# Optimization experiments

Measured on AMD Instinct MI355X. Metric: run time of the kernel, lower is better.

## Reference

```python
import jax, jax.numpy as jnp
import numpy as np

N, E, B = 4096, 4096, 128  # nodes, edges, graphs


def _param(key, shape, scale):
    return jax.random.normal(key, shape, dtype=jnp.float32) * scale


def setup_inputs() -> dict:
    key = jax.random.key(0)
    ks = jax.random.split(key, 32)
    inp = {
        "x": jax.random.normal(ks[0], (N, 37), dtype=jnp.float32),
        "edge_index": jax.random.randint(ks[1], (2, E), 0, N),
        "edge_attr": jax.random.uniform(ks[2], (E, 5), dtype=jnp.float32),
        "batch": jnp.sort(jax.random.randint(ks[3], (N,), 0, B)),
        # NNConv 1: edge-MLP 5->512->37*128, root [37,128]
        "nn1_w1": _param(ks[4], (5, 512), 0.3),
        "nn1_b1": jnp.zeros((512,), jnp.float32),
        "nn1_w2": _param(ks[5], (512, 37 * 128), 0.01),
        "nn1_b2": jnp.zeros((37 * 128,), jnp.float32),
        "root1": _param(ks[6], (37, 128), 0.1),
        "bias1": jnp.zeros((128,), jnp.float32),
        # NNConv 2: edge-MLP 5->128->128*256, root [128,256]
        "nn2_w1": _param(ks[7], (5, 128), 0.3),
        "nn2_b1": jnp.zeros((128,), jnp.float32),
        "nn2_w2": _param(ks[8], (128, 128 * 256), 0.005),
        "nn2_b2": jnp.zeros((128 * 256,), jnp.float32),
        "root2": _param(ks[9], (128, 256), 0.05),
        "bias2": jnp.zeros((256,), jnp.float32),
        # NNConv 3: edge-MLP 5->128->256*256, root [256,256]
        "nn3_w1": _param(ks[10], (5, 128), 0.3),
        "nn3_b1": jnp.zeros((128,), jnp.float32),
        "nn3_w2": _param(ks[11], (128, 256 * 256), 0.005),
        "nn3_b2": jnp.zeros((256 * 256,), jnp.float32),
        "root3": _param(ks[12], (256, 256), 0.05),
        "bias3": jnp.zeros((256,), jnp.float32),
        # readout MLP
        "fc1_w": _param(ks[13], (256, 128), 0.06),
        "fc1_b": jnp.zeros((128,), jnp.float32),
        "fc2_w": _param(ks[14], (128, 64), 0.09),
        "fc2_b": jnp.zeros((64,), jnp.float32),
        "fc3_w": _param(ks[15], (64, 1), 0.12),
        "fc3_b": jnp.zeros((1,), jnp.float32),
    }
    return inp


def _nnconv(x, src, dst, edge_attr, w1, b1, w2, b2, root, bias, cin, cout):
    # edge MLP -> per-edge weight matrix [E, cin, cout]
    h = jax.nn.relu(edge_attr @ w1 + b1)
    W = (h @ w2 + b2).reshape(-1, cin, cout)
    # gather source features, per-edge matvec, scatter-add to targets
    msg = jnp.einsum('ei,eio->eo', x[src], W)          # [E, cout]
    agg = jax.ops.segment_sum(msg, dst, num_segments=x.shape[0])
    return agg + x @ root + bias


def _segment_mean(x, seg, num_segments):
    s = jax.ops.segment_sum(x, seg, num_segments=num_segments)
    cnt = jax.ops.segment_sum(jnp.ones((x.shape[0],), x.dtype), seg,
                              num_segments=num_segments)
    return s / jnp.maximum(cnt, 1.0)[:, None]


def reference(x, edge_index, edge_attr, batch,
              nn1_w1, nn1_b1, nn1_w2, nn1_b2, root1, bias1,
              nn2_w1, nn2_b1, nn2_w2, nn2_b2, root2, bias2,
              nn3_w1, nn3_b1, nn3_w2, nn3_b2, root3, bias3,
              fc1_w, fc1_b, fc2_w, fc2_b, fc3_w, fc3_b):
    src, dst = edge_index[0], edge_index[1]
    h = jax.nn.elu(_nnconv(x, src, dst, edge_attr, nn1_w1, nn1_b1, nn1_w2,
                           nn1_b2, root1, bias1, 37, 128))
    h = jax.nn.elu(_nnconv(h, src, dst, edge_attr, nn2_w1, nn2_b1, nn2_w2,
                           nn2_b2, root2, bias2, 128, 256))
    h = jax.nn.elu(_nnconv(h, src, dst, edge_attr, nn3_w1, nn3_b1, nn3_w2,
                           nn3_b2, root3, bias3, 256, 256))
    g = _segment_mean(h, batch, B)                     # [B, 256]
    g = jax.nn.elu(g @ fc1_w + fc1_b)
    g = jax.nn.elu(g @ fc2_w + fc2_b)
    g = g @ fc3_w + fc3_b
    return g.reshape(-1)
```

## Files before the change

### kernel.cpp

```cpp
#include <hip/hip_runtime.h>
#include <cstdint>
#include <cstddef>

typedef float f32x4 __attribute__((ext_vector_type(4)));
typedef _Float16 f16x8 __attribute__((ext_vector_type(8)));
typedef _Float16 f16x4 __attribute__((ext_vector_type(4)));

__device__ __forceinline__ float elu_f(float x) { return x > 0.f ? x : expm1f(x); }

__device__ __forceinline__ void gload_lds16(const void* g, void* l)
{
    __builtin_amdgcn_global_load_lds(
        (const __attribute__((address_space(1))) void*)g,
        (__attribute__((address_space(3))) void*)l,
        16, 0, 0);
}

template <int CIN, int COUT, int KFTOT>
__device__ __forceinline__
void pack_body(int bid, int tid, const float* __restrict__ w2, const float* __restrict__ b2,
               _Float16* __restrict__ w2h, int KH, float* tile )
{
    const int kh = bid / KFTOT;
    const int c  = bid - kh * KFTOT;
    const int CP = 32 * COUT;
    for (int i = tid; i < CP; i += 256) {
        int kk = i / COUT, n = i - kk * COUT;
        int kg = c * 32 + kk;
        float v = 0.f;
        if (kg < CIN) v = (kh < KH) ? w2[((size_t)kh * CIN + kg) * COUT + n]
                                    : b2[(size_t)kg * COUT + n];
        tile[kk * (COUT + 2) + n] = v;
    }
    __syncthreads();
    _Float16* outp = w2h + (size_t)bid * CP;
    for (int i = tid; i < CP; i += 256) {
        int n = i >> 5, kk = i & 31;
        int blk = (kk >> 3) ^ ((n >> 1) & 3);
        outp[n * 32 + blk * 8 + (kk & 7)] = (_Float16)tile[kk * (COUT + 2) + n];
    }
}

__global__ __launch_bounds__(256)
void uber_prologue_kernel(const float* __restrict__ ea,
                          const int* __restrict__ dst, int* __restrict__ cnt,
                          const float* __restrict__ w1a, const float* __restrict__ b1a, _Float16* __restrict__ h1T,
                          const float* __restrict__ w1b, const float* __restrict__ b1b, _Float16* __restrict__ h2T,
                          const float* __restrict__ w1c, const float* __restrict__ b1c, _Float16* __restrict__ h3T,
                          int E,
                          const float* __restrict__ w2a, const float* __restrict__ b2a, _Float16* __restrict__ w2h1,
                          const float* __restrict__ w2b, const float* __restrict__ b2b, _Float16* __restrict__ w2h2,
                          const float* __restrict__ w2c, const float* __restrict__ b2c, _Float16* __restrict__ w2h3)
{
    __shared__ __align__(16) float smem[32 * 258];
    const int tid = threadIdx.x;
    const int nEB = E >> 6;
    int b = blockIdx.x;

    if (b < nEB) {
        const int e0 = b * 64;
        const int el = tid & 63;
        const int cg = tid >> 6;
        if (tid < 64) atomicAdd(&cnt[dst[e0 + tid]], 1);
        float* a = smem;
        for (int i = tid; i < 320; i += 256) a[(i / 5) * 5 + (i % 5)] = ea[e0 * 5 + i];
        __syncthreads();
        float av[5];
        #pragma unroll
        for (int j = 0; j < 5; ++j) av[j] = a[el * 5 + j];
        #pragma unroll 4
        for (int t = 0; t < 128; ++t) {
            const int ch = t * 4 + cg;
            float s = b1a[ch];
            #pragma unroll
            for (int j = 0; j < 5; ++j) s = fmaf(av[j], w1a[j * 512 + ch], s);
            h1T[(size_t)ch * E + e0 + el] = (_Float16)fmaxf(s, 0.f);
        }
        #pragma unroll 4
        for (int t = 0; t < 32; ++t) {
            const int ch = t * 4 + cg;
            float s = b1b[ch];
            float u = b1c[ch];
            #pragma unroll
            for (int j = 0; j < 5; ++j) {
                s = fmaf(av[j], w1b[j * 128 + ch], s);
                u = fmaf(av[j], w1c[j * 128 + ch], u);
            }
            h2T[(size_t)ch * E + e0 + el] = (_Float16)fmaxf(s, 0.f);
            h3T[(size_t)ch * E + e0 + el] = (_Float16)fmaxf(u, 0.f);
        }
        return;
    }
    b -= nEB;
    if (b < 513 * 2) { pack_body<37, 128, 2>(b, tid, w2a, b2a, w2h1, 512, smem); return; }
    b -= 513 * 2;
    if (b < 129 * 4) { pack_body<128, 256, 4>(b, tid, w2b, b2b, w2h2, 128, smem); return; }
    b -= 129 * 4;
    pack_body<256, 256, 8>(b, tid, w2c, b2c, w2h3, 128, smem);
}

__global__ __launch_bounds__(256)
void csr_scan_graph_kernel(const int* __restrict__ cnt, int* __restrict__ offs, int N,
                           const int* __restrict__ batch, int* __restrict__ goffs, int B,
                           int NN)
{
    __shared__ int sums[256];
    __shared__ int pref[257];
    const int tid = threadIdx.x;
    const int per = N / 256;
    int loc = 0;
    for (int i = 0; i < per; ++i) loc += cnt[tid * per + i];
    sums[tid] = loc;
    __syncthreads();
    if (tid == 0) {
        int s = 0; pref[0] = 0;
        for (int i = 0; i < 256; ++i) { s += sums[i]; pref[i + 1] = s; }
    }
    __syncthreads();
    int run = pref[tid];
    for (int i = 0; i < per; ++i) { offs[tid * per + i] = run; run += cnt[tid * per + i]; }
    if (tid == 255) offs[N] = run;
    for (int g = tid; g <= B; g += 256) {
        int lo = 0, hi = NN;
        while (lo < hi) { int mid = (lo + hi) >> 1; if (batch[mid] < g) lo = mid + 1; else hi = mid; }
        goffs[g] = lo;
    }
}

__global__ __launch_bounds__(256)
void csr_fill_kernel(const int* __restrict__ dst, const int* __restrict__ offs,
                     int* __restrict__ cur, int* __restrict__ eid, int E)
{
    int e = blockIdx.x * 256 + threadIdx.x;
    if (e < E) {
        int d = dst[e];
        int p = offs[d] + atomicAdd(&cur[d], 1);
        eid[p] = e;
    }
}

template <int KH, int CIN, int COUT, int KFTOT, int CSPLIT, int NY>
__global__ __launch_bounds__(256, 4)
void msg_mfma_kernel(const float* __restrict__ xin,
                     const _Float16* __restrict__ hT,
                     const _Float16* __restrict__ w2h,
                     const int* __restrict__ src,
                     _Float16* __restrict__ part,
                     int E, int khg_per)
{
    constexpr int BM = 256;
    constexpr int KF = KFTOT / CSPLIT;

    __shared__ __align__(16) _Float16 bsh[3][KF][64][32];
    __shared__ int s_src[BM];

    const int tid  = threadIdx.x;
    const int lane = tid & 63;
    const int w    = tid >> 6;
    const int l15  = lane & 15;
    const int lg   = lane >> 4;
    const int swb  = (l15 >> 1) & 3;

    const int nwg = gridDim.x;
    const int bid = blockIdx.x;
    const int swz = (bid & 7) * (nwg >> 3) + (bid >> 3);
    const int m    = swz & 15;
    const int rest = swz >> 4;
    const int y    = rest % NY;
    const int zz   = rest / NY;
    const int cinH = zz % CSPLIT;
    const int zkh  = zz / CSPLIT;

    const int e0  = m * BM;
    const int n0  = y * 64;
    const int k0  = cinH * KF * 32;
    const int kh0 = zkh * khg_per;
    const int kh1 = min(kh0 + khg_per, KH + 1);

    s_src[tid] = src[e0 + tid];
    __syncthreads();

    f16x8 a_[4][KF];
    #pragma unroll
    for (int mf = 0; mf < 4; ++mf) {
        const int eloc = w * 64 + mf * 16 + l15;
        const float* xrow = xin + (size_t)s_src[eloc] * CIN + k0;
        #pragma unroll
        for (int c = 0; c < KF; ++c) {
            if (CIN % 32 == 0) {
                float4 p0 = *(const float4*)(xrow + c * 32 + lg * 8);
                float4 p1 = *(const float4*)(xrow + c * 32 + lg * 8 + 4);
                a_[mf][c][0] = (_Float16)p0.x; a_[mf][c][1] = (_Float16)p0.y;
                a_[mf][c][2] = (_Float16)p0.z; a_[mf][c][3] = (_Float16)p0.w;
                a_[mf][c][4] = (_Float16)p1.x; a_[mf][c][5] = (_Float16)p1.y;
                a_[mf][c][6] = (_Float16)p1.z; a_[mf][c][7] = (_Float16)p1.w;
            } else {
                #pragma unroll
                for (int j = 0; j < 8; ++j) {
                    int kk = c * 32 + lg * 8 + j;
                    float v = (k0 + kk < CIN) ? xrow[kk] : 0.f;
                    a_[mf][c][j] = (_Float16)v;
                }
            }
        }
    }

    f32x4 msg[4][4];
    #pragma unroll
    for (int mf = 0; mf < 4; ++mf)
        #pragma unroll
        for (int nf = 0; nf < 4; ++nf) msg[mf][nf] = 0.f;

    auto stage = [&](int khg, int pp) {
        if (khg >= kh1) return;
        const size_t chunk0 = (size_t)khg * KFTOT + cinH * KF;
        const char* g = (const char*)(w2h + (chunk0 * COUT + n0) * 32) + (size_t)tid * 16;
        char* l = (char*)(&bsh[pp][0][0][0]) + (tid >> 6) * 1024;
        #pragma unroll
        for (int c = 0; c < KF; ++c)
            gload_lds16(g + (size_t)c * COUT * 64, l + c * 4096);
    };

    stage(kh0, 0);
    stage(kh0 + 1, 1);

    int bi = 0;
    for (int khg = kh0; khg < kh1; ++khg) {
        asm volatile("s_waitcnt vmcnt(2)" ::: "memory");
        __builtin_amdgcn_s_barrier();

        _Float16 hh[4];
        if (khg < KH) {
            const _Float16* hp = hT + (size_t)khg * E + e0 + w * 64 + l15;
            #pragma unroll
            for (int mf = 0; mf < 4; ++mf) hh[mf] = hp[mf * 16];
        } else {
            #pragma unroll
            for (int mf = 0; mf < 4; ++mf) hh[mf] = (_Float16)1.0f;
        }
        __builtin_amdgcn_sched_barrier(0);

        int bi2 = bi + 2; if (bi2 >= 3) bi2 -= 3;
        stage(khg + 2, bi2);

        __builtin_amdgcn_s_setprio(1);
        #pragma unroll
        for (int c = 0; c < KF; ++c) {
            f16x8 Bv[4];
            #pragma unroll
            for (int nf = 0; nf < 4; ++nf)
                Bv[nf] = *(const f16x8*)&bsh[bi][c][nf * 16 + l15][(lg ^ swb) * 8];
            #pragma unroll
            for (int mf = 0; mf < 4; ++mf) {
                f16x8 ah = a_[mf][c] * hh[mf];
                #pragma unroll
                for (int nf = 0; nf < 4; ++nf)
                    msg[mf][nf] = __builtin_amdgcn_mfma_f32_16x16x32_f16(ah, Bv[nf], msg[mf][nf], 0, 0, 0);
            }
        }
        __builtin_amdgcn_s_setprio(0);

        ++bi; if (bi == 3) bi = 0;
    }

    _Float16* pb = part + ((size_t)zz * E + e0) * COUT + n0;
    #pragma unroll
    for (int mf = 0; mf < 4; ++mf)
        #pragma unroll
        for (int r = 0; r < 4; ++r) {
            const int row = w * 64 + mf * 16 + lg * 4 + r;
            #pragma unroll
            for (int nf = 0; nf < 4; ++nf)
                pb[(size_t)row * COUT + nf * 16 + l15] = (_Float16)msg[mf][nf][r];
        }
}

template <int CIN, int COUT, int Z>
__global__ __launch_bounds__(256)
void node_gemm_kernel(const float* __restrict__ xin,
                      const float* __restrict__ root,
                      const _Float16* __restrict__ part,
                      const int* __restrict__ offs,
                      const int* __restrict__ eid,
                      const float* __restrict__ bias,
                      float* __restrict__ out, int E)
{
    constexpr int BM  = 32;
    constexpr int BN  = 64;
    constexpr int BKI = (CIN % 32 == 0) ? 32 : 16;
    constexpr int CIN_PAD = ((CIN + BKI - 1) / BKI) * BKI;
    constexpr int CPK = CIN_PAD / BKI;
    constexpr int NROWS = BKI / 16;

    __shared__ __align__(16) float xs_t[CIN_PAD][BM];
    __shared__ __align__(16) float btile[BKI][BN];

    const int tid = threadIdx.x;
    const int tx  = tid & 15;
    const int ty  = tid >> 4;
    const int ty2 = ty * 2;
    const int tx4 = tx * 4;
    const int e0  = blockIdx.x * BM;
    const int n0  = blockIdx.y * BN;

    for (int idx = tid; idx < BM * CIN_PAD; idx += 256) {
        int mm = idx / CIN_PAD;
        int i  = idx - mm * CIN_PAD;
        float v = 0.f;
        if (i < CIN) v = xin[(size_t)(e0 + mm) * CIN + i];
        xs_t[i][mm] = v;
    }

    const int rbase = tid >> 4;
    const int nn    = (tid & 15) * 4;
    float acc[2][4] = {};
    float4 pre[NROWS];

    {
        const float* brow = root + n0;
        #pragma unroll
        for (int rr = 0; rr < NROWS; ++rr) {
            int r = rbase + rr * 16;
            float4 v = {0.f, 0.f, 0.f, 0.f};
            if (r < CIN) v = *(const float4*)(brow + (size_t)r * COUT + nn);
            pre[rr] = v;
        }
    }

    for (int c = 0; c < CPK; ++c) {
        __syncthreads();
        #pragma unroll
        for (int rr = 0; rr < NROWS; ++rr)
            *(float4*)&btile[rbase + rr * 16][nn] = pre[rr];
        __syncthreads();

        if (c + 1 < CPK) {
            int i0n = (c + 1) * BKI;
            const float* brow = root + (size_t)i0n * COUT + n0;
            #pragma unroll
            for (int rr = 0; rr < NROWS; ++rr) {
                int r = rbase + rr * 16;
                float4 v = {0.f, 0.f, 0.f, 0.f};
                if (i0n + r < CIN) v = *(const float4*)(brow + (size_t)r * COUT + nn);
                pre[rr] = v;
            }
        }

        const int i0 = c * BKI;
        #pragma unroll
        for (int ii = 0; ii < BKI; ++ii) {
            float2 xv = *(const float2*)&xs_t[i0 + ii][ty2];
            float4 bv = *(const float4*)&btile[ii][tx4];
            float av[2] = {xv.x, xv.y};
            float bvv[4] = {bv.x, bv.y, bv.z, bv.w};
            #pragma unroll
            for (int mm = 0; mm < 2; ++mm)
                #pragma unroll
                for (int nq = 0; nq < 4; ++nq)
                    acc[mm][nq] = fmaf(av[mm], bvv[nq], acc[mm][nq]);
        }
    }

    float bs[4];
    #pragma unroll
    for (int nq = 0; nq < 4; ++nq) bs[nq] = bias[n0 + tx4 + nq];

    #pragma unroll
    for (int mm = 0; mm < 2; ++mm) {
        const int row = e0 + ty2 + mm;
        float add[4] = {0.f, 0.f, 0.f, 0.f};
        const int b = offs[row], t = offs[row + 1];
        for (int j = b; j < t; ++j) {
            const int e = eid[j];
            #pragma unroll
            for (int z = 0; z < Z; ++z) {
                f16x4 r4 = *(const f16x4*)(part + ((size_t)z * E + e) * COUT + n0 + tx4);
                add[0] += (float)r4.x; add[1] += (float)r4.y;
                add[2] += (float)r4.z; add[3] += (float)r4.w;
            }
        }
        size_t base = (size_t)row * COUT + n0 + tx4;
        #pragma unroll
        for (int nq = 0; nq < 4; ++nq)
            out[base + nq] = elu_f(acc[mm][nq] + add[nq] + bs[nq]);
    }
}

__global__ __launch_bounds__(256)
void pool_readout_kernel(const float* __restrict__ hl3, const int* __restrict__ goffs,
                         const float* __restrict__ fc1w, const float* __restrict__ fc1b,
                         const float* __restrict__ fc2w, const float* __restrict__ fc2b,
                         const float* __restrict__ fc3w, const float* __restrict__ fc3b,
                         float* __restrict__ outp)
{
    const int g   = blockIdx.x;
    const int tid = threadIdx.x;
    __shared__ float gm[256];
    __shared__ float a1[128];
    __shared__ float a2[64];
    const int b = goffs[g], t = goffs[g + 1];
    float s = 0.f;
    for (int n = b; n < t; ++n) s += hl3[(size_t)n * 256 + tid];
    gm[tid] = s / fmaxf((float)(t - b), 1.f);
    __syncthreads();
    if (tid < 128) {
        float v = fc1b[tid];
        for (int j = 0; j < 256; ++j) v = fmaf(gm[j], fc1w[j * 128 + tid], v);
        a1[tid] = elu_f(v);
    }
    __syncthreads();
    if (tid < 64) {
        float v = fc2b[tid];
        for (int j = 0; j < 128; ++j) v = fmaf(a1[j], fc2w[j * 64 + tid], v);
        a2[tid] = elu_f(v);
    }
    __syncthreads();
    if (tid == 0) {
        float v = fc3b[0];
        for (int j = 0; j < 64; ++j) v = fmaf(a2[j], fc3w[j], v);
        outp[g] = v;
    }
}

extern "C" void kernel_launch(void* const* d_in, const int* in_sizes, int n_in,
                              void* d_out, int out_size, void* d_ws, size_t ws_size,
                              hipStream_t stream)
{
    const float* x      = (const float*)d_in[0];
    const int*   ei     = (const int*)  d_in[1];
    const float* ea     = (const float*)d_in[2];
    const int*   batch  = (const int*)  d_in[3];
    const float* nn1_w1 = (const float*)d_in[4];
    const float* nn1_b1 = (const float*)d_in[5];
    const float* nn1_w2 = (const float*)d_in[6];
    const float* nn1_b2 = (const float*)d_in[7];
    const float* root1  = (const float*)d_in[8];
    const float* bias1  = (const float*)d_in[9];
    const float* nn2_w1 = (const float*)d_in[10];
    const float* nn2_b1 = (const float*)d_in[11];
    const float* nn2_w2 = (const float*)d_in[12];
    const float* nn2_b2 = (const float*)d_in[13];
    const float* root2  = (const float*)d_in[14];
    const float* bias2  = (const float*)d_in[15];
    const float* nn3_w1 = (const float*)d_in[16];
    const float* nn3_b1 = (const float*)d_in[17];
    const float* nn3_w2 = (const float*)d_in[18];
    const float* nn3_b2 = (const float*)d_in[19];
    const float* root3  = (const float*)d_in[20];
    const float* bias3  = (const float*)d_in[21];
    const float* fc1_w  = (const float*)d_in[22];
    const float* fc1_b  = (const float*)d_in[23];
    const float* fc2_w  = (const float*)d_in[24];
    const float* fc2_b  = (const float*)d_in[25];
    const float* fc3_w  = (const float*)d_in[26];
    const float* fc3_b  = (const float*)d_in[27];

    const int E = in_sizes[2] / 5;
    const int N = in_sizes[0] / 37;
    const int B = out_size;
    const int* srcp = ei;
    const int* dstp = ei + E;

    const size_t W1H = (size_t)513 * 2 * 128 * 32;
    const size_t W2H = (size_t)129 * 4 * 256 * 32;
    const size_t W3H = (size_t)129 * 8 * 256 * 32;
    _Float16* w2h1 = (_Float16*)d_ws;
    _Float16* w2h2 = w2h1 + W1H;
    _Float16* w2h3 = w2h2 + W2H;
    _Float16* h1T  = w2h3 + W3H;
    _Float16* h2T  = h1T + (size_t)512 * E;
    _Float16* h3T  = h2T + (size_t)128 * E;
    _Float16* part = h3T + (size_t)128 * E;
    float* fbase = (float*)(part + (size_t)32 * E * 128);
    float* hl1   = fbase;
    float* hl2   = hl1 + (size_t)N * 128;
    float* hl3   = hl2 + (size_t)N * 256;
    int* ibase   = (int*)(hl3 + (size_t)N * 256);
    int* cnt   = ibase;
    int* cur   = cnt + N;
    int* offs  = cur + N;
    int* eid   = offs + N + 1;
    int* goffs = eid + E;

    hipMemsetAsync(cnt, 0, 2 * N * sizeof(int), stream);

    const int nEB = E / 64;
    uber_prologue_kernel<<<nEB + 1026 + 516 + 1032, 256, 0, stream>>>(
        ea, dstp, cnt,
        nn1_w1, nn1_b1, h1T, nn2_w1, nn2_b1, h2T, nn3_w1, nn3_b1, h3T, E,
        nn1_w2, nn1_b2, w2h1, nn2_w2, nn2_b2, w2h2, nn3_w2, nn3_b2, w2h3);

    csr_scan_graph_kernel<<<1, 256, 0, stream>>>(cnt, offs, N, batch, goffs, B, N);
    csr_fill_kernel<<<(E + 255) / 256, 256, 0, stream>>>(dstp, offs, cur, eid, E);

    msg_mfma_kernel<512, 37, 128, 2, 1, 2><<<1024, 256, 0, stream>>>(
        x, h1T, w2h1, srcp, part, E, 17);
    node_gemm_kernel<37, 128, 32><<<dim3(N / 32, 2), 256, 0, stream>>>(
        x, root1, part, offs, eid, bias1, hl1, E);

    msg_mfma_kernel<128, 128, 256, 4, 2, 4><<<1024, 256, 0, stream>>>(
        hl1, h2T, w2h2, srcp, part, E, 17);
    node_gemm_kernel<128, 256, 16><<<dim3(N / 32, 4), 256, 0, stream>>>(
        hl1, root2, part, offs, eid, bias2, hl2, E);

    msg_mfma_kernel<128, 256, 256, 8, 4, 4><<<1024, 256, 0, stream>>>(
        hl2, h3T, w2h3, srcp, part, E, 33);
    node_gemm_kernel<256, 256, 16><<<dim3(N / 32, 4), 256, 0, stream>>>(
        hl2, root3, part, offs, eid, bias3, hl3, E);

    pool_readout_kernel<<<B, 256, 0, stream>>>(hl3, goffs, fc1_w, fc1_b,
                                               fc2_w, fc2_b, fc3_w, fc3_b,
                                               (float*)d_out);
}
```

Baseline: 304.4 us.

## Restructure message MFMA pipeline into double-buffered pairs of K-chunks

The message kernel's weight staging moves from a three-slot ring with one chunk per iteration to two buffers that each hold two K-chunks. The loop now advances two chunks per step and synchronises once per pair with __syncthreads. The aim is to halve the barrier count and give the asynchronous LDS loads a longer compute window to overlap with. In exchange, shared memory per block grows from three to four chunk slots, which could lower occupancy, and the s_setprio hints and the fine-grained vmcnt wait are removed.

After: 994.3 us. +226.6%, slower.

```diff
diff --git a/kernel.cpp b/kernel.cpp
--- a/kernel.cpp
+++ b/kernel.cpp
@@ -151,7 +151,7 @@
     constexpr int BM = 256;
     constexpr int KF = KFTOT / CSPLIT;
 
-    __shared__ __align__(16) _Float16 bsh[3][KF][64][32];
+    __shared__ __align__(16) _Float16 bsh[2][2][KF][64][32];
     __shared__ int s_src[BM];
 
     const int tid  = threadIdx.x;
@@ -211,56 +211,59 @@
         #pragma unroll
         for (int nf = 0; nf < 4; ++nf) msg[mf][nf] = 0.f;
 
-    auto stage = [&](int khg, int pp) {
+    auto stage = [&](int khg, int pp, int sub) {
         if (khg >= kh1) return;
         const size_t chunk0 = (size_t)khg * KFTOT + cinH * KF;
         const char* g = (const char*)(w2h + (chunk0 * COUT + n0) * 32) + (size_t)tid * 16;
-        char* l = (char*)(&bsh[pp][0][0][0]) + (tid >> 6) * 1024;
+        char* l = (char*)(&bsh[pp][sub][0][0][0]) + (tid >> 6) * 1024;
         #pragma unroll
         for (int c = 0; c < KF; ++c)
             gload_lds16(g + (size_t)c * COUT * 64, l + c * 4096);
     };
 
-    stage(kh0, 0);
-    stage(kh0 + 1, 1);
-
-    int bi = 0;
-    for (int khg = kh0; khg < kh1; ++khg) {
-        asm volatile("s_waitcnt vmcnt(2)" ::: "memory");
-        __builtin_amdgcn_s_barrier();
-
-        _Float16 hh[4];
-        if (khg < KH) {
-            const _Float16* hp = hT + (size_t)khg * E + e0 + w * 64 + l15;
-            #pragma unroll
-            for (int mf = 0; mf < 4; ++mf) hh[mf] = hp[mf * 16];
-        } else {
-            #pragma unroll
-            for (int mf = 0; mf < 4; ++mf) hh[mf] = (_Float16)1.0f;
-        }
-        __builtin_amdgcn_sched_barrier(0);
-
-        int bi2 = bi + 2; if (bi2 >= 3) bi2 -= 3;
-        stage(khg + 2, bi2);
-
-        __builtin_amdgcn_s_setprio(1);
-        #pragma unroll
-        for (int c = 0; c < KF; ++c) {
-            f16x8 Bv[4];
-            #pragma unroll
-            for (int nf = 0; nf < 4; ++nf)
-                Bv[nf] = *(const f16x8*)&bsh[bi][c][nf * 16 + l15][(lg ^ swb) * 8];
-            #pragma unroll
-            for (int mf = 0; mf < 4; ++mf) {
-                f16x8 ah = a_[mf][c] * hh[mf];
+    stage(kh0, 0, 0);
+    stage(kh0 + 1, 0, 1);
+
+    int p = 0;
+    for (int kb = kh0; kb < kh1; kb += 2) {
+        __syncthreads();
+
+        stage(kb + 2, p ^ 1, 0);
+        stage(kb + 3, p ^ 1, 1);
+
+        _Float16 hh[2][4];
+        #pragma unroll
+        for (int sub = 0; sub < 2; ++sub) {
+            const int kh = kb + sub;
+            if (kh < kh1 && kh < KH) {
+                const _Float16* hp = hT + (size_t)kh * E + e0 + w * 64 + l15;
+                #pragma unroll
+                for (int mf = 0; mf < 4; ++mf) hh[sub][mf] = hp[mf * 16];
+            } else {
+                #pragma unroll
+                for (int mf = 0; mf < 4; ++mf) hh[sub][mf] = (_Float16)1.0f;
+            }
+        }
+
+        #pragma unroll
+        for (int sub = 0; sub < 2; ++sub) {
+            if (kb + sub >= kh1) break;
+            #pragma unroll
+            for (int c = 0; c < KF; ++c) {
+                f16x8 Bv[4];
                 #pragma unroll
                 for (int nf = 0; nf < 4; ++nf)
-                    msg[mf][nf] = __builtin_amdgcn_mfma_f32_16x16x32_f16(ah, Bv[nf], msg[mf][nf], 0, 0, 0);
+                    Bv[nf] = *(const f16x8*)&bsh[p][sub][c][nf * 16 + l15][(lg ^ swb) * 8];
+                #pragma unroll
+                for (int mf = 0; mf < 4; ++mf) {
+                    f16x8 ah = a_[mf][c] * hh[sub][mf];
+                    #pragma unroll
+                    for (int nf = 0; nf < 4; ++nf)
+                        msg[mf][nf] = __builtin_amdgcn_mfma_f32_16x16x32_f16(ah, Bv[nf], msg[mf][nf], 0, 0, 0);
+                }
             }
         }
-        __builtin_amdgcn_s_setprio(0);
-
-        ++bi; if (bi == 3) bi = 0;
+        p ^= 1;
     }
 
     _Float16* pb = part + ((size_t)zz * E + e0) * COUT + n0;
```
